# Kernel tuning notes

Hardware: AMD Instinct MI355X
Metric: run time of the kernel (lower is better)

The kernel has to match this reference:

```python
import jax, jax.numpy as jnp
import numpy as np

B, S, N, H, F, L, Lt = 2, 8, 150, 128, 40, 2, 1
EF = 2 * F + 2  # 82: src feat + dst feat + distance + bond
_rows_np, _cols_np = np.where(~np.eye(N, dtype=bool))  # fully connected, no self loops
_rows = jnp.asarray(_rows_np)
_cols = jnp.asarray(_cols_np)
E = _rows_np.shape[0]


def setup_inputs() -> dict:
    key = jax.random.key(0)
    ks = jax.random.split(key, 20)
    w = lambda k, shape: 0.1 * jax.random.normal(k, shape, dtype=jnp.float32)
    d = {}
    d['t'] = jax.random.uniform(ks[0], (B, 1), dtype=jnp.float32)
    d['x'] = jax.random.normal(ks[1], (B, S, N, 3), dtype=jnp.float32)
    d['peptide_seq'] = jax.random.randint(ks[2], (B, 15), 0, 20)
    d['atom_labels'] = jax.random.randint(ks[3], (B, N), 0, 5)
    d['amino_acid_pos'] = jax.random.randint(ks[4], (B, N), 1, 16)
    d['bond_matrix'] = (jax.random.uniform(ks[5], (B, N, N)) < 0.1).astype(jnp.float32)
    d['edge_mask'] = jnp.ones((B, N, N), jnp.float32)
    d['atom_mask'] = jnp.ones((B, N, 1), jnp.float32)
    d['restore_indices'] = jnp.tile(jnp.eye(N, dtype=jnp.float32)[None], (B, 1, 1))
    d['W_e1'] = w(ks[6], (L, EF, H)); d['b_e1'] = jnp.zeros((L, H), jnp.float32)
    d['W_e2'] = w(ks[7], (L, H, H)); d['b_e2'] = jnp.zeros((L, H), jnp.float32)
    d['W_c'] = w(ks[8], (L, H, 1)); d['b_c'] = jnp.zeros((L, 1), jnp.float32)
    d['W_h'] = w(ks[9], (L, F + H, F)); d['b_h'] = jnp.zeros((L, F), jnp.float32)
    d['w_t'] = w(ks[10], (L, 1, H)); d['w_b_t'] = jnp.zeros((L, H), jnp.float32)
    d['tW_e1'] = w(ks[11], (Lt, EF, H)); d['tb_e1'] = jnp.zeros((Lt, H), jnp.float32)
    d['tW_e2'] = w(ks[12], (Lt, H, H)); d['tb_e2'] = jnp.zeros((Lt, H), jnp.float32)
    d['tW_c'] = w(ks[13], (Lt, H, 1)); d['tb_c'] = jnp.zeros((Lt, 1), jnp.float32)
    d['tW_h'] = w(ks[14], (Lt, F + H, F)); d['tb_h'] = jnp.zeros((Lt, F), jnp.float32)
    return d


def _forward(t, x, peptide_seq, atom_labels, amino_acid_pos, bond_matrix, edge_mask,
             atom_mask, restore_indices, W_e1, b_e1, W_e2, b_e2, W_c, b_c, W_h, b_h,
             w_t, w_b_t, tW_e1, tb_e1, tW_e2, tb_e2, tW_c, tb_c, tW_h, tb_h):
    # single-atom embedding: [B, N, 40]
    aa = jnp.take_along_axis(peptide_seq, amino_acid_pos - 1, axis=1)
    emb = jnp.concatenate([
        jax.nn.one_hot(atom_labels, 5, dtype=x.dtype),
        jax.nn.one_hot(aa, 20, dtype=x.dtype),
        jax.nn.one_hot(amino_acid_pos - 1, 15, dtype=x.dtype)], axis=-1)
    h = jnp.broadcast_to(emb[:, None], (B, S, N, F))
    # restore absolute coordinates: x[b,s,i,d] = sum_j x[b,s,j,d] * R[b,i,j]
    x = jnp.einsum('bsjd,bij->bsid', x, restore_indices)
    x0 = x
    # per-edge masks/features (gathered once; identical math to full cdist + indexing)
    em_e = edge_mask.reshape(B, 1, N * N)[:, :, _rows * N + _cols][..., None]  # [B,1,E,1]
    bond_e = jnp.broadcast_to(bond_matrix[:, _rows, _cols][:, None, :, None], (B, S, E, 1))

    def layer(x, h, We1, be1, We2, be2, Wc, bc, Wh, bh, temb):
        diff = x[:, :, _rows] - x[:, :, _cols]                      # [B,S,E,3]
        dist = jnp.sqrt(jnp.sum(diff * diff, -1, keepdims=True) + 1e-12)
        ef = jnp.concatenate([h[:, :, _rows], h[:, :, _cols], dist, bond_e], -1)  # [B,S,E,82]
        m = jax.nn.silu(ef @ We1 + be1 + temb)
        m = jax.nn.silu(m @ We2 + be2) * em_e                        # [B,S,E,H]
        cw = m @ Wc + bc                                             # [B,S,E,1]
        x_out = jnp.zeros_like(x).at[:, :, _rows].add(diff * cw) / (N - 1)
        agg = jnp.zeros((B, S, N, m.shape[-1]), m.dtype).at[:, :, _rows].add(m)
        h_out = jax.nn.silu(jnp.concatenate([h, agg], -1) @ Wh + bh)
        return x_out, h_out

    for l in range(L):
        temb = (t @ w_t[l] + w_b_t[l])[:, None, None, :]             # [B,1,1,H]
        xo, h = layer(x, h, W_e1[l], b_e1[l], W_e2[l], b_e2[l], W_c[l], b_c[l], W_h[l], b_h[l], temb)
        x = x + xo
    for l in range(Lt):
        xo, h = layer(x, h, tW_e1[l], tb_e1[l], tW_e2[l], tb_e2[l], tW_c[l], tb_c[l], tW_h[l], tb_h[l], 0.0)
        x = x + xo
    return (x - x0) * atom_mask[:, None, :, :]


def reference(t, x, peptide_seq, atom_labels, amino_acid_pos, bond_matrix, edge_mask,
              atom_mask, restore_indices, W_e1, b_e1, W_e2, b_e2, W_c, b_c, W_h, b_h,
              w_t, w_b_t, tW_e1, tb_e1, tW_e2, tb_e2, tW_c, tb_c, tW_h, tb_h):
    return _forward(t, x, peptide_seq, atom_labels, amino_acid_pos, bond_matrix, edge_mask,
                    atom_mask, restore_indices, W_e1, b_e1, W_e2, b_e2, W_c, b_c, W_h, b_h,
                    w_t, w_b_t, tW_e1, tb_e1, tW_e2, tb_e2, tW_c, tb_c, tW_h, tb_h)
```

## Files before the change

### kernel.cpp

```cpp
#include <hip/hip_runtime.h>
#include <math.h>

#define B_ 2
#define S_ 8
#define N_ 150
#define H_ 128
#define F_ 40
#define EF_ 82
#define NP_ 160
#define MPQ 136

typedef __attribute__((ext_vector_type(8))) short short8;
typedef __attribute__((ext_vector_type(4))) float float4v;

__device__ __forceinline__ float silu_f(float v) {
    return v * __builtin_amdgcn_rcpf(1.0f + __expf(-v));
}

__device__ __forceinline__ unsigned short f2bf(float f) {
    unsigned u = __builtin_bit_cast(unsigned, f);
    return (unsigned short)((u + 0x7fffu + ((u >> 16) & 1u)) >> 16);
}

__global__ void pack_we2_kernel(const float* __restrict__ w0,
                                const float* __restrict__ w1,
                                const float* __restrict__ w2,
                                unsigned short* __restrict__ outp) {
    int e = blockIdx.x * blockDim.x + threadIdx.x;
    int l = e >> 14, idx = e & 16383;
    int k = idx >> 7, c = idx & 127;
    const float* src = (l == 0) ? w0 : (l == 1) ? w1 : w2;
    outp[l * 16384 + c * H_ + k] = f2bf(src[idx]);
}

__global__ void restore_x_kernel(const float* __restrict__ x,
                                 const float* __restrict__ R,
                                 float* __restrict__ xa,
                                 float* __restrict__ x0) {
    int idx = blockIdx.x * blockDim.x + threadIdx.x;
    if (idx >= B_ * S_ * N_ * 3) return;
    int d = idx % 3;
    int i = (idx / 3) % N_;
    int bs = idx / (3 * N_);
    int b = bs / S_;
    const float* xrow = x + bs * N_ * 3 + d;
    const float* Rrow = R + (b * N_ + i) * N_;
    float acc = 0.0f;
    for (int j = 0; j < N_; j++) acc += xrow[j * 3] * Rrow[j];
    xa[idx] = acc;
    x0[idx] = acc;
}

__global__ void node0_kernel(const int* __restrict__ pep,
                             const int* __restrict__ labels,
                             const int* __restrict__ aapos,
                             const float* __restrict__ We1,
                             const float* __restrict__ be1,
                             const float* __restrict__ tp,
                             const float* __restrict__ wt,
                             const float* __restrict__ wbt,
                             float* __restrict__ h0,
                             float* __restrict__ Af,
                             float* __restrict__ Bf) {
    int bi = blockIdx.x;
    int b = bi / N_, i = bi % N_;
    int c = threadIdx.x;
    int al = labels[bi];
    int ap = aapos[bi];
    int aa = pep[b * 15 + ap - 1];
    int r0 = al, r1 = 5 + aa, r2 = 25 + ap - 1;
    float fa = We1[r0 * H_ + c] + We1[r1 * H_ + c] + We1[r2 * H_ + c]
             + be1[c] + tp[b] * wt[c] + wbt[c];
    float fb = We1[(F_ + r0) * H_ + c] + We1[(F_ + r1) * H_ + c] + We1[(F_ + r2) * H_ + c];
    float hv = 0.0f;
    if (c < F_) hv = (c == r0 || c == r1 || c == r2) ? 1.0f : 0.0f;
    for (int s = 0; s < S_; s++) {
        int n = (b * S_ + s) * N_ + i;
        Af[n * H_ + c] = fa;
        Bf[n * H_ + c] = fb;
        if (c < F_) h0[n * F_ + c] = hv;
    }
}

__global__ void node_kernel(const float* __restrict__ h_in,
                            const float* __restrict__ agg,
                            const float* __restrict__ Wh,
                            const float* __restrict__ bh,
                            const float* __restrict__ We1n,
                            const float* __restrict__ be1n,
                            const float* __restrict__ tp,
                            const float* __restrict__ wtn,
                            const float* __restrict__ wbtn,
                            int has_t,
                            float* __restrict__ h_out,
                            float* __restrict__ Af,
                            float* __restrict__ Bf) {
    int n = blockIdx.x;
    int b = n / (S_ * N_);
    int tid = threadIdx.x;
    __shared__ float cat[F_ + H_];
    __shared__ float part[120];
    __shared__ float hnew[F_];
    if (tid < F_) cat[tid] = h_in[n * F_ + tid];
    cat[F_ + tid] = agg[n * H_ + tid];
    __syncthreads();
    if (tid < 120) {
        int f = tid % 40, ks = tid / 40;
        float p = 0.0f;
        int k0 = ks * 56;
#pragma unroll 8
        for (int k = k0; k < k0 + 56; k++) p += cat[k] * Wh[k * F_ + f];
        part[tid] = p;
    }
    __syncthreads();
    if (tid < F_) {
        float hv = silu_f(part[tid] + part[40 + tid] + part[80 + tid] + bh[tid]);
        hnew[tid] = hv;
        h_out[n * F_ + tid] = hv;
    }
    __syncthreads();
    float fa = be1n[tid] + (has_t ? tp[b] * wtn[tid] + wbtn[tid] : 0.0f);
    float fb = 0.0f;
#pragma unroll 8
    for (int k = 0; k < F_; k++) {
        float hv = hnew[k];
        fa += hv * We1n[k * H_ + tid];
        fb += hv * We1n[(F_ + k) * H_ + tid];
    }
    Af[n * H_ + tid] = fa;
    Bf[n * H_ + tid] = fb;
}

__global__ __launch_bounds__(256, 4) void edge_kernel(
    const float* __restrict__ x_in,
    const float* __restrict__ Afeat,
    const float* __restrict__ Bfeat,
    const float* __restrict__ We1,
    const unsigned short* __restrict__ we2t,
    const float* __restrict__ be2,
    const float* __restrict__ Wc,
    const float* __restrict__ bcp,
    const float* __restrict__ bond,
    const float* __restrict__ emask,
    const float* __restrict__ x0v,
    const float* __restrict__ amask,
    int final_mode,
    float* __restrict__ x_out,
    float* __restrict__ agg_out)
{
    __shared__ __align__(16) short mbuf[2][16 * MPQ];
    __shared__ float4 diffE[NP_];
    __shared__ float2 dbL[NP_];
    __shared__ float DsumL[3];
    __shared__ float wpart[4][3];

    int blk = blockIdx.x;
    int i = blk % N_, bs = blk / N_, b = bs / S_;
    int tid = threadIdx.x;
    int node = bs * N_ + i;
    int lane = tid & 63, w = tid >> 6;
    int qd = lane >> 4, l15 = lane & 15;
    int rowLoc = tid >> 4, c0 = (tid & 15) * 8;

    float xi0 = x_in[node * 3 + 0];
    float xi1 = x_in[node * 3 + 1];
    float xi2 = x_in[node * 3 + 2];

    if (tid < NP_) {
        int j = tid;
        float xj0 = xi0, xj1 = xi1, xj2 = xi2, bnd = 0.0f, emv = 0.0f;
        if (j < N_) {
            int nj = bs * N_ + j;
            xj0 = x_in[nj * 3 + 0];
            xj1 = x_in[nj * 3 + 1];
            xj2 = x_in[nj * 3 + 2];
            int eij = (b * N_ + i) * N_ + j;
            bnd = bond[eij];
            emv = (j == i) ? 0.0f : emask[eij];
        }
        float d0 = xi0 - xj0, d1 = xi1 - xj1, d2 = xi2 - xj2;
        diffE[j] = make_float4(d0, d1, d2, emv);
        dbL[j] = make_float2(sqrtf(d0 * d0 + d1 * d1 + d2 * d2 + 1e-12f), bnd);
    }

    float afr[8], w80r[8], w81r[8];
    {
        float4 t0 = *(const float4*)&Afeat[node * H_ + c0];
        float4 t1 = *(const float4*)&Afeat[node * H_ + c0 + 4];
        afr[0]=t0.x; afr[1]=t0.y; afr[2]=t0.z; afr[3]=t0.w;
        afr[4]=t1.x; afr[5]=t1.y; afr[6]=t1.z; afr[7]=t1.w;
        t0 = *(const float4*)&We1[80 * H_ + c0];
        t1 = *(const float4*)&We1[80 * H_ + c0 + 4];
        w80r[0]=t0.x; w80r[1]=t0.y; w80r[2]=t0.z; w80r[3]=t0.w;
        w80r[4]=t1.x; w80r[5]=t1.y; w80r[6]=t1.z; w80r[7]=t1.w;
        t0 = *(const float4*)&We1[81 * H_ + c0];
        t1 = *(const float4*)&We1[81 * H_ + c0 + 4];
        w81r[0]=t0.x; w81r[1]=t0.y; w81r[2]=t0.z; w81r[3]=t0.w;
        w81r[4]=t1.x; w81r[5]=t1.y; w81r[6]=t1.z; w81r[7]=t1.w;
    }

    int ctb = w * 2;
    float b2r0 = be2[ctb * 16 + l15],  b2r1 = be2[ctb * 16 + 16 + l15];
    float wc0  = Wc[ctb * 16 + l15],   wc1  = Wc[ctb * 16 + 16 + l15];
    const unsigned short* bb0 = we2t + (ctb * 16 + l15) * H_ + qd * 8;
    const unsigned short* bb1 = bb0 + 16 * H_;
    short8 bf00 = *(const short8*)(bb0 +  0);
    short8 bf01 = *(const short8*)(bb0 + 32);
    short8 bf02 = *(const short8*)(bb0 + 64);
    short8 bf03 = *(const short8*)(bb0 + 96);
    short8 bf10 = *(const short8*)(bb1 +  0);
    short8 bf11 = *(const short8*)(bb1 + 32);
    short8 bf12 = *(const short8*)(bb1 + 64);
    short8 bf13 = *(const short8*)(bb1 + 96);

    __syncthreads();

    if (w == 0) {
        float p0 = 0, p1 = 0, p2 = 0;
        for (int j = lane; j < NP_; j += 64) {
            float4 d = diffE[j];
            p0 += d.x; p1 += d.y; p2 += d.z;
        }
        for (int s = 1; s < 64; s <<= 1) {
            p0 += __shfl_xor(p0, s, 64);
            p1 += __shfl_xor(p1, s, 64);
            p2 += __shfl_xor(p2, s, 64);
        }
        if (lane == 0) { DsumL[0] = p0; DsumL[1] = p1; DsumL[2] = p2; }
    }

    float aggP0 = 0, aggP1 = 0;
    float SP00 = 0, SP01 = 0, SP02 = 0, SP10 = 0, SP11 = 0, SP12 = 0;

    for (int jt = 0; jt < 10; jt++) {
        short* mb = mbuf[jt & 1];
        int jrow = jt * 16 + rowLoc;
        float mv[8];
        if (jrow < N_) {
            const float* bp = &Bfeat[(bs * N_ + jrow) * H_ + c0];
            float4 b0 = *(const float4*)bp;
            float4 b1 = *(const float4*)(bp + 4);
            float br[8] = {b0.x, b0.y, b0.z, b0.w, b1.x, b1.y, b1.z, b1.w};
            float2 db = dbL[jrow];
#pragma unroll
            for (int u = 0; u < 8; u++)
                mv[u] = silu_f(afr[u] + br[u] + db.x * w80r[u] + db.y * w81r[u]);
        } else {
#pragma unroll
            for (int u = 0; u < 8; u++) mv[u] = 0.0f;
        }
        short8 pkv;
#pragma unroll
        for (int u = 0; u < 8; u++) pkv[u] = (short)f2bf(mv[u]);
        *(short8*)&mb[rowLoc * MPQ + c0] = pkv;
        __syncthreads();

        const short* arow = &mb[l15 * MPQ + qd * 8];
        short8 a0 = *(const short8*)(arow +  0);
        short8 a1 = *(const short8*)(arow + 32);
        short8 a2 = *(const short8*)(arow + 64);
        short8 a3 = *(const short8*)(arow + 96);
        float4v acc0 = {0, 0, 0, 0}, acc1 = {0, 0, 0, 0};
        acc0 = __builtin_amdgcn_mfma_f32_16x16x32_bf16(a0, bf00, acc0, 0, 0, 0);
        acc1 = __builtin_amdgcn_mfma_f32_16x16x32_bf16(a0, bf10, acc1, 0, 0, 0);
        acc0 = __builtin_amdgcn_mfma_f32_16x16x32_bf16(a1, bf01, acc0, 0, 0, 0);
        acc1 = __builtin_amdgcn_mfma_f32_16x16x32_bf16(a1, bf11, acc1, 0, 0, 0);
        acc0 = __builtin_amdgcn_mfma_f32_16x16x32_bf16(a2, bf02, acc0, 0, 0, 0);
        acc1 = __builtin_amdgcn_mfma_f32_16x16x32_bf16(a2, bf12, acc1, 0, 0, 0);
        acc0 = __builtin_amdgcn_mfma_f32_16x16x32_bf16(a3, bf03, acc0, 0, 0, 0);
        acc1 = __builtin_amdgcn_mfma_f32_16x16x32_bf16(a3, bf13, acc1, 0, 0, 0);

#pragma unroll
        for (int r = 0; r < 4; r++) {
            int j = jt * 16 + qd * 4 + r;
            float4 de = diffE[j];
            float mv0 = silu_f(acc0[r] + b2r0) * de.w;
            float mv1 = silu_f(acc1[r] + b2r1) * de.w;
            aggP0 += mv0; aggP1 += mv1;
            SP00 += de.x * mv0; SP01 += de.y * mv0; SP02 += de.z * mv0;
            SP10 += de.x * mv1; SP11 += de.y * mv1; SP12 += de.z * mv1;
        }
    }

#define QR_(v) { v += __shfl_xor(v, 16, 64); v += __shfl_xor(v, 32, 64); }
    QR_(aggP0) QR_(aggP1)
    QR_(SP00) QR_(SP01) QR_(SP02)
    QR_(SP10) QR_(SP11) QR_(SP12)
#undef QR_

    if (!final_mode && qd == 0) {
        agg_out[node * H_ + ctb * 16 + l15]      = aggP0;
        agg_out[node * H_ + ctb * 16 + 16 + l15] = aggP1;
    }

    float p0 = wc0 * SP00 + wc1 * SP10;
    float p1 = wc0 * SP01 + wc1 * SP11;
    float p2 = wc0 * SP02 + wc1 * SP12;
    for (int s = 1; s < 16; s <<= 1) {
        p0 += __shfl_xor(p0, s, 64);
        p1 += __shfl_xor(p1, s, 64);
        p2 += __shfl_xor(p2, s, 64);
    }
    if (lane == 0) { wpart[w][0] = p0; wpart[w][1] = p1; wpart[w][2] = p2; }
    __syncthreads();
    if (tid < 3) {
        float tot = wpart[0][tid] + wpart[1][tid] + wpart[2][tid] + wpart[3][tid]
                  + bcp[0] * DsumL[tid];
        float xn = x_in[node * 3 + tid] + tot * (1.0f / (float)(N_ - 1));
        if (final_mode)
            x_out[node * 3 + tid] = (xn - x0v[node * 3 + tid]) * amask[b * N_ + i];
        else
            x_out[node * 3 + tid] = xn;
    }
}

extern "C" void kernel_launch(void* const* d_in, const int* in_sizes, int n_in,
                              void* d_out, int out_size, void* d_ws, size_t ws_size,
                              hipStream_t stream) {
    const float* t     = (const float*)d_in[0];
    const float* x     = (const float*)d_in[1];
    const int*   pep   = (const int*)d_in[2];
    const int*   labels= (const int*)d_in[3];
    const int*   aapos = (const int*)d_in[4];
    const float* bond  = (const float*)d_in[5];
    const float* em    = (const float*)d_in[6];
    const float* amask = (const float*)d_in[7];
    const float* R     = (const float*)d_in[8];
    const float* W_e1  = (const float*)d_in[9];
    const float* b_e1  = (const float*)d_in[10];
    const float* W_e2  = (const float*)d_in[11];
    const float* b_e2  = (const float*)d_in[12];
    const float* W_c   = (const float*)d_in[13];
    const float* b_c   = (const float*)d_in[14];
    const float* W_h   = (const float*)d_in[15];
    const float* b_h   = (const float*)d_in[16];
    const float* w_t   = (const float*)d_in[17];
    const float* w_b_t = (const float*)d_in[18];
    const float* tW_e1 = (const float*)d_in[19];
    const float* tb_e1 = (const float*)d_in[20];
    const float* tW_e2 = (const float*)d_in[21];
    const float* tb_e2 = (const float*)d_in[22];
    const float* tW_c  = (const float*)d_in[23];
    const float* tb_c  = (const float*)d_in[24];
    float* out = (float*)d_out;

    float* ws = (float*)d_ws;
    unsigned short* we2t = (unsigned short*)ws;
    float* x0  = ws + 24576;
    float* xA  = x0 + 7200;
    float* xB  = xA + 7200;
    float* hA  = xB + 7200;
    float* hB  = hA + 96000;
    float* agg = hB + 96000;
    float* Af  = agg + 307200;
    float* Bf  = Af + 307200;

    const int XE = B_ * S_ * N_ * 3;
    const int NB = B_ * S_ * N_;

    pack_we2_kernel<<<48, 1024, 0, stream>>>(W_e2, W_e2 + H_ * H_, tW_e2, we2t);
    restore_x_kernel<<<(XE + 255) / 256, 256, 0, stream>>>(x, R, xA, x0);
    node0_kernel<<<B_ * N_, H_, 0, stream>>>(pep, labels, aapos, W_e1, b_e1,
                                             t, w_t, w_b_t, hA, Af, Bf);

    edge_kernel<<<NB, 256, 0, stream>>>(xA, Af, Bf, W_e1, we2t, b_e2, W_c, b_c,
                                        bond, em, nullptr, nullptr, 0, xB, agg);
    node_kernel<<<NB, H_, 0, stream>>>(hA, agg, W_h, b_h,
                                       W_e1 + EF_ * H_, b_e1 + H_,
                                       t, w_t + H_, w_b_t + H_, 1, hB, Af, Bf);

    edge_kernel<<<NB, 256, 0, stream>>>(xB, Af, Bf, W_e1 + EF_ * H_, we2t + 16384,
                                        b_e2 + H_, W_c + H_, b_c + 1,
                                        bond, em, nullptr, nullptr, 0, xA, agg);
    node_kernel<<<NB, H_, 0, stream>>>(hB, agg, W_h + (F_ + H_) * F_, b_h + F_,
                                       tW_e1, tb_e1,
                                       nullptr, nullptr, nullptr, 0, hA, Af, Bf);

    edge_kernel<<<NB, 256, 0, stream>>>(xA, Af, Bf, tW_e1, we2t + 32768,
                                        tb_e2, tW_c, tb_c,
                                        bond, em, x0, amask, 1, out, agg);
}
```

Before: 277.0 us.

## Fuse node update into edge kernel, merge prep kernels, software-pipeline message tiles

Merges the three setup kernels into one prep launch and folds the node MLP (h update and next-layer A/B feature projection) into the tail of each edge kernel. This removes the agg round trip through global memory and several launches. Af/Bf are now double-buffered so that one block's writes cannot race with other blocks still reading the current layer. The edge loop is also software-pipelined: the next 16-row message tile is computed while the MFMAs for the current tile run, leaving one barrier per iteration. The cost is more shared memory and registers per edge block, which may lower occupancy.

```diff
diff --git a/kernel.cpp b/kernel.cpp
--- a/kernel.cpp
+++ b/kernel.cpp
@@ -22,113 +22,63 @@
     return (unsigned short)((u + 0x7fffu + ((u >> 16) & 1u)) >> 16);
 }
 
-__global__ void pack_we2_kernel(const float* __restrict__ w0,
-                                const float* __restrict__ w1,
-                                const float* __restrict__ w2,
-                                unsigned short* __restrict__ outp) {
-    int e = blockIdx.x * blockDim.x + threadIdx.x;
-    int l = e >> 14, idx = e & 16383;
-    int k = idx >> 7, c = idx & 127;
-    const float* src = (l == 0) ? w0 : (l == 1) ? w1 : w2;
-    outp[l * 16384 + c * H_ + k] = f2bf(src[idx]);
-}
-
-__global__ void restore_x_kernel(const float* __restrict__ x,
-                                 const float* __restrict__ R,
-                                 float* __restrict__ xa,
-                                 float* __restrict__ x0) {
-    int idx = blockIdx.x * blockDim.x + threadIdx.x;
-    if (idx >= B_ * S_ * N_ * 3) return;
-    int d = idx % 3;
-    int i = (idx / 3) % N_;
-    int bs = idx / (3 * N_);
-    int b = bs / S_;
-    const float* xrow = x + bs * N_ * 3 + d;
-    const float* Rrow = R + (b * N_ + i) * N_;
-    float acc = 0.0f;
-    for (int j = 0; j < N_; j++) acc += xrow[j * 3] * Rrow[j];
-    xa[idx] = acc;
-    x0[idx] = acc;
-}
-
-__global__ void node0_kernel(const int* __restrict__ pep,
-                             const int* __restrict__ labels,
-                             const int* __restrict__ aapos,
-                             const float* __restrict__ We1,
-                             const float* __restrict__ be1,
-                             const float* __restrict__ tp,
-                             const float* __restrict__ wt,
-                             const float* __restrict__ wbt,
-                             float* __restrict__ h0,
-                             float* __restrict__ Af,
-                             float* __restrict__ Bf) {
-    int bi = blockIdx.x;
-    int b = bi / N_, i = bi % N_;
-    int c = threadIdx.x;
-    int al = labels[bi];
-    int ap = aapos[bi];
-    int aa = pep[b * 15 + ap - 1];
-    int r0 = al, r1 = 5 + aa, r2 = 25 + ap - 1;
-    float fa = We1[r0 * H_ + c] + We1[r1 * H_ + c] + We1[r2 * H_ + c]
-             + be1[c] + tp[b] * wt[c] + wbt[c];
-    float fb = We1[(F_ + r0) * H_ + c] + We1[(F_ + r1) * H_ + c] + We1[(F_ + r2) * H_ + c];
-    float hv = 0.0f;
-    if (c < F_) hv = (c == r0 || c == r1 || c == r2) ? 1.0f : 0.0f;
-    for (int s = 0; s < S_; s++) {
-        int n = (b * S_ + s) * N_ + i;
-        Af[n * H_ + c] = fa;
-        Bf[n * H_ + c] = fb;
-        if (c < F_) h0[n * F_ + c] = hv;
-    }
-}
-
-__global__ void node_kernel(const float* __restrict__ h_in,
-                            const float* __restrict__ agg,
-                            const float* __restrict__ Wh,
-                            const float* __restrict__ bh,
-                            const float* __restrict__ We1n,
-                            const float* __restrict__ be1n,
-                            const float* __restrict__ tp,
-                            const float* __restrict__ wtn,
-                            const float* __restrict__ wbtn,
-                            int has_t,
-                            float* __restrict__ h_out,
-                            float* __restrict__ Af,
-                            float* __restrict__ Bf) {
-    int n = blockIdx.x;
-    int b = n / (S_ * N_);
+__global__ __launch_bounds__(512) void prep_kernel(
+    const float* __restrict__ x, const float* __restrict__ R,
+    const int* __restrict__ pep, const int* __restrict__ labels,
+    const int* __restrict__ aapos,
+    const float* __restrict__ We1, const float* __restrict__ be1,
+    const float* __restrict__ tp, const float* __restrict__ wt,
+    const float* __restrict__ wbt,
+    const float* __restrict__ w2a, const float* __restrict__ w2b,
+    const float* __restrict__ w2c,
+    unsigned short* __restrict__ we2t,
+    float* __restrict__ xa, float* __restrict__ x0,
+    float* __restrict__ h0, float* __restrict__ Af, float* __restrict__ Bf)
+{
+    int blk = blockIdx.x;
     int tid = threadIdx.x;
-    __shared__ float cat[F_ + H_];
-    __shared__ float part[120];
-    __shared__ float hnew[F_];
-    if (tid < F_) cat[tid] = h_in[n * F_ + tid];
-    cat[F_ + tid] = agg[n * H_ + tid];
-    __syncthreads();
-    if (tid < 120) {
-        int f = tid % 40, ks = tid / 40;
-        float p = 0.0f;
-        int k0 = ks * 56;
-#pragma unroll 8
-        for (int k = k0; k < k0 + 56; k++) p += cat[k] * Wh[k * F_ + f];
-        part[tid] = p;
-    }
-    __syncthreads();
-    if (tid < F_) {
-        float hv = silu_f(part[tid] + part[40 + tid] + part[80 + tid] + bh[tid]);
-        hnew[tid] = hv;
-        h_out[n * F_ + tid] = hv;
-    }
-    __syncthreads();
-    float fa = be1n[tid] + (has_t ? tp[b] * wtn[tid] + wbtn[tid] : 0.0f);
-    float fb = 0.0f;
-#pragma unroll 8
-    for (int k = 0; k < F_; k++) {
-        float hv = hnew[k];
-        fa += hv * We1n[k * H_ + tid];
-        fb += hv * We1n[(F_ + k) * H_ + tid];
-    }
-    Af[n * H_ + tid] = fa;
-    Bf[n * H_ + tid] = fb;
+    if (blk < 96) {
+        int e = blk * 512 + tid;
+        int l = e >> 14, idx = e & 16383;
+        int k = idx >> 7, c = idx & 127;
+        const float* src = (l == 0) ? w2a : (l == 1) ? w2b : w2c;
+        we2t[l * 16384 + c * H_ + k] = f2bf(src[idx]);
+    } else if (blk < 112) {
+        int bs = blk - 96;
+        int b = bs / S_;
+        __shared__ float xL[N_ * 3];
+        if (tid < N_ * 3) xL[tid] = x[bs * N_ * 3 + tid];
+        __syncthreads();
+        if (tid < N_ * 3) {
+            int i = tid / 3, d = tid % 3;
+            const float* Rrow = R + (b * N_ + i) * N_;
+            float acc = 0.0f;
+#pragma unroll 5
+            for (int j = 0; j < N_; j++) acc += xL[j * 3 + d] * Rrow[j];
+            xa[bs * N_ * 3 + tid] = acc;
+            x0[bs * N_ * 3 + tid] = acc;
+        }
+    } else {
+        int sub = tid >> 7, c = tid & 127;
+        int bi = (blk - 112) * 4 + sub;
+        int b = bi / N_, i = bi % N_;
+        int al = labels[bi];
+        int ap = aapos[bi];
+        int aa = pep[b * 15 + ap - 1];
+        int r0 = al, r1 = 5 + aa, r2 = 25 + ap - 1;
+        float fa = We1[r0 * H_ + c] + We1[r1 * H_ + c] + We1[r2 * H_ + c]
+                 + be1[c] + tp[b] * wt[c] + wbt[c];
+        float fb = We1[(F_ + r0) * H_ + c] + We1[(F_ + r1) * H_ + c]
+                 + We1[(F_ + r2) * H_ + c];
+        float hv = 0.0f;
+        if (c < F_) hv = (c == r0 || c == r1 || c == r2) ? 1.0f : 0.0f;
+        for (int s = 0; s < S_; s++) {
+            int n = (b * S_ + s) * N_ + i;
+            Af[n * H_ + c] = fa;
+            Bf[n * H_ + c] = fb;
+            if (c < F_) h0[n * F_ + c] = hv;
+        }
+    }
 }
 
 __global__ __launch_bounds__(256, 4) void edge_kernel(
@@ -142,17 +92,31 @@
     const float* __restrict__ bcp,
     const float* __restrict__ bond,
     const float* __restrict__ emask,
+    const float* __restrict__ h_in,
+    const float* __restrict__ Wh,
+    const float* __restrict__ bh,
+    const float* __restrict__ We1n,
+    const float* __restrict__ be1n,
+    const float* __restrict__ tpn,
+    const float* __restrict__ wtn,
+    const float* __restrict__ wbtn,
+    int has_t_next,
     const float* __restrict__ x0v,
     const float* __restrict__ amask,
     int final_mode,
     float* __restrict__ x_out,
-    float* __restrict__ agg_out)
+    float* __restrict__ h_out,
+    float* __restrict__ Af_out,
+    float* __restrict__ Bf_out)
 {
     __shared__ __align__(16) short mbuf[2][16 * MPQ];
     __shared__ float4 diffE[NP_];
     __shared__ float2 dbL[NP_];
     __shared__ float DsumL[3];
     __shared__ float wpart[4][3];
+    __shared__ float cat[F_ + H_];
+    __shared__ float part[160];
+    __shared__ float hnewL[F_];
 
     int blk = blockIdx.x;
     int i = blk % N_, bs = blk / N_, b = bs / S_;
@@ -229,37 +193,40 @@
         if (lane == 0) { DsumL[0] = p0; DsumL[1] = p1; DsumL[2] = p2; }
     }
 
+    {
+        const float* bp = &Bfeat[(bs * N_ + rowLoc) * H_ + c0];
+        float4 b0 = *(const float4*)bp;
+        float4 b1 = *(const float4*)(bp + 4);
+        float br[8] = {b0.x, b0.y, b0.z, b0.w, b1.x, b1.y, b1.z, b1.w};
+        float2 db = dbL[rowLoc];
+        short8 pkv;
+#pragma unroll
+        for (int u = 0; u < 8; u++)
+            pkv[u] = (short)f2bf(silu_f(afr[u] + br[u] + db.x * w80r[u] + db.y * w81r[u]));
+        *(short8*)&mbuf[0][rowLoc * MPQ + c0] = pkv;
+    }
+    __syncthreads();
+
     float aggP0 = 0, aggP1 = 0;
     float SP00 = 0, SP01 = 0, SP02 = 0, SP10 = 0, SP11 = 0, SP12 = 0;
 
+#pragma unroll 2
     for (int jt = 0; jt < 10; jt++) {
         short* mb = mbuf[jt & 1];
-        int jrow = jt * 16 + rowLoc;
-        float mv[8];
-        if (jrow < N_) {
-            const float* bp = &Bfeat[(bs * N_ + jrow) * H_ + c0];
-            float4 b0 = *(const float4*)bp;
-            float4 b1 = *(const float4*)(bp + 4);
-            float br[8] = {b0.x, b0.y, b0.z, b0.w, b1.x, b1.y, b1.z, b1.w};
-            float2 db = dbL[jrow];
-#pragma unroll
-            for (int u = 0; u < 8; u++)
-                mv[u] = silu_f(afr[u] + br[u] + db.x * w80r[u] + db.y * w81r[u]);
-        } else {
-#pragma unroll
-            for (int u = 0; u < 8; u++) mv[u] = 0.0f;
-        }
-        short8 pkv;
-#pragma unroll
-        for (int u = 0; u < 8; u++) pkv[u] = (short)f2bf(mv[u]);
-        *(short8*)&mb[rowLoc * MPQ + c0] = pkv;
-        __syncthreads();
-
         const short* arow = &mb[l15 * MPQ + qd * 8];
         short8 a0 = *(const short8*)(arow +  0);
         short8 a1 = *(const short8*)(arow + 32);
         short8 a2 = *(const short8*)(arow + 64);
         short8 a3 = *(const short8*)(arow + 96);
+
+        int jr = jt * 16 + 16 + rowLoc;
+        float4 nb0 = {0,0,0,0}, nb1 = {0,0,0,0};
+        if (jt < 9 && jr < N_) {
+            const float* bp = &Bfeat[(bs * N_ + jr) * H_ + c0];
+            nb0 = *(const float4*)bp;
+            nb1 = *(const float4*)(bp + 4);
+        }
+
         float4v acc0 = {0, 0, 0, 0}, acc1 = {0, 0, 0, 0};
         acc0 = __builtin_amdgcn_mfma_f32_16x16x32_bf16(a0, bf00, acc0, 0, 0, 0);
         acc1 = __builtin_amdgcn_mfma_f32_16x16x32_bf16(a0, bf10, acc1, 0, 0, 0);
@@ -270,6 +237,21 @@
         acc0 = __builtin_amdgcn_mfma_f32_16x16x32_bf16(a3, bf03, acc0, 0, 0, 0);
         acc1 = __builtin_amdgcn_mfma_f32_16x16x32_bf16(a3, bf13, acc1, 0, 0, 0);
 
+        if (jt < 9) {
+            short8 pkv;
+            if (jr < N_) {
+                float br[8] = {nb0.x, nb0.y, nb0.z, nb0.w, nb1.x, nb1.y, nb1.z, nb1.w};
+                float2 db = dbL[jr];
+#pragma unroll
+                for (int u = 0; u < 8; u++)
+                    pkv[u] = (short)f2bf(silu_f(afr[u] + br[u] + db.x * w80r[u] + db.y * w81r[u]));
+            } else {
+#pragma unroll
+                for (int u = 0; u < 8; u++) pkv[u] = 0;
+            }
+            *(short8*)&mbuf[(jt + 1) & 1][rowLoc * MPQ + c0] = pkv;
+        }
+
 #pragma unroll
         for (int r = 0; r < 4; r++) {
             int j = jt * 16 + qd * 4 + r;
@@ -280,6 +262,7 @@
             SP00 += de.x * mv0; SP01 += de.y * mv0; SP02 += de.z * mv0;
             SP10 += de.x * mv1; SP11 += de.y * mv1; SP12 += de.z * mv1;
         }
+        __syncthreads();
     }
 
 #define QR_(v) { v += __shfl_xor(v, 16, 64); v += __shfl_xor(v, 32, 64); }
@@ -287,11 +270,6 @@
     QR_(SP00) QR_(SP01) QR_(SP02)
     QR_(SP10) QR_(SP11) QR_(SP12)
 #undef QR_
-
-    if (!final_mode && qd == 0) {
-        agg_out[node * H_ + ctb * 16 + l15]      = aggP0;
-        agg_out[node * H_ + ctb * 16 + 16 + l15] = aggP1;
-    }
 
     float p0 = wc0 * SP00 + wc1 * SP10;
     float p1 = wc0 * SP01 + wc1 * SP11;
@@ -302,6 +280,13 @@
         p2 += __shfl_xor(p2, s, 64);
     }
     if (lane == 0) { wpart[w][0] = p0; wpart[w][1] = p1; wpart[w][2] = p2; }
+    if (!final_mode) {
+        if (qd == 0) {
+            cat[F_ + ctb * 16 + l15]      = aggP0;
+            cat[F_ + ctb * 16 + 16 + l15] = aggP1;
+        }
+        if (tid < F_) cat[tid] = h_in[node * F_ + tid];
+    }
     __syncthreads();
     if (tid < 3) {
         float tot = wpart[0][tid] + wpart[1][tid] + wpart[2][tid] + wpart[3][tid]
@@ -311,6 +296,37 @@
             x_out[node * 3 + tid] = (xn - x0v[node * 3 + tid]) * amask[b * N_ + i];
         else
             x_out[node * 3 + tid] = xn;
+    }
+    if (final_mode) return;
+
+    if (tid < 160) {
+        int f = tid >> 2, ks = tid & 3;
+        int k0 = ks * 42;
+        float p = 0.0f;
+#pragma unroll 6
+        for (int k = k0; k < k0 + 42; k++) p += cat[k] * Wh[k * F_ + f];
+        part[tid] = p;
+    }
+    __syncthreads();
+    if (tid < F_) {
+        float hv = silu_f(part[tid * 4] + part[tid * 4 + 1] + part[tid * 4 + 2]
+                        + part[tid * 4 + 3] + bh[tid]);
+        hnewL[tid] = hv;
+        h_out[node * F_ + tid] = hv;
+    }
+    __syncthreads();
+    {
+        int c = tid & 127, grp = tid >> 7;
+        float acc = 0.0f;
+        if (grp == 0) {
+            acc = be1n[c];
+            if (has_t_next) acc += tpn[b] * wtn[c] + wbtn[c];
+        }
+        const float* Wp = We1n + grp * F_ * H_ + c;
+#pragma unroll 8
+        for (int k = 0; k < F_; k++) acc += hnewL[k] * Wp[k * H_];
+        if (grp == 0) Af_out[node * H_ + c] = acc;
+        else          Bf_out[node * H_ + c] = acc;
     }
 }
 
@@ -351,32 +367,33 @@
     float* xB  = xA + 7200;
     float* hA  = xB + 7200;
     float* hB  = hA + 96000;
-    float* agg = hB + 96000;
-    float* Af  = agg + 307200;
-    float* Bf  = Af + 307200;
-
-    const int XE = B_ * S_ * N_ * 3;
+    float* AfA = hB + 96000;
+    float* BfA = AfA + 307200;
+    float* AfB = BfA + 307200;
+    float* BfB = AfB + 307200;
+
     const int NB = B_ * S_ * N_;
 
-    pack_we2_kernel<<<48, 1024, 0, stream>>>(W_e2, W_e2 + H_ * H_, tW_e2, we2t);
-    restore_x_kernel<<<(XE + 255) / 256, 256, 0, stream>>>(x, R, xA, x0);
-    node0_kernel<<<B_ * N_, H_, 0, stream>>>(pep, labels, aapos, W_e1, b_e1,
-                                             t, w_t, w_b_t, hA, Af, Bf);
-
-    edge_kernel<<<NB, 256, 0, stream>>>(xA, Af, Bf, W_e1, we2t, b_e2, W_c, b_c,
-                                        bond, em, nullptr, nullptr, 0, xB, agg);
-    node_kernel<<<NB, H_, 0, stream>>>(hA, agg, W_h, b_h,
-                                       W_e1 + EF_ * H_, b_e1 + H_,
-                                       t, w_t + H_, w_b_t + H_, 1, hB, Af, Bf);
-
-    edge_kernel<<<NB, 256, 0, stream>>>(xB, Af, Bf, W_e1 + EF_ * H_, we2t + 16384,
-                                        b_e2 + H_, W_c + H_, b_c + 1,
-                                        bond, em, nullptr, nullptr, 0, xA, agg);
-    node_kernel<<<NB, H_, 0, stream>>>(hB, agg, W_h + (F_ + H_) * F_, b_h + F_,
-                                       tW_e1, tb_e1,
-                                       nullptr, nullptr, nullptr, 0, hA, Af, Bf);
-
-    edge_kernel<<<NB, 256, 0, stream>>>(xA, Af, Bf, tW_e1, we2t + 32768,
-                                        tb_e2, tW_c, tb_c,
-                                        bond, em, x0, amask, 1, out, agg);
-}
+    prep_kernel<<<187, 512, 0, stream>>>(x, R, pep, labels, aapos,
+                                         W_e1, b_e1, t, w_t, w_b_t,
+                                         W_e2, W_e2 + H_ * H_, tW_e2,
+                                         we2t, xA, x0, hA, AfA, BfA);
+
+    edge_kernel<<<NB, 256, 0, stream>>>(xA, AfA, BfA, W_e1, we2t, b_e2, W_c, b_c,
+        bond, em,
+        hA, W_h, b_h, W_e1 + EF_ * H_, b_e1 + H_, t, w_t + H_, w_b_t + H_, 1,
+        nullptr, nullptr, 0,
+        xB, hB, AfB, BfB);
+
+    edge_kernel<<<NB, 256, 0, stream>>>(xB, AfB, BfB, W_e1 + EF_ * H_, we2t + 16384,
+        b_e2 + H_, W_c + H_, b_c + 1, bond, em,
+        hB, W_h + (F_ + H_) * F_, b_h + F_, tW_e1, tb_e1, nullptr, nullptr, nullptr, 0,
+        nullptr, nullptr, 0,
+        xA, hA, AfA, BfA);
+
+    edge_kernel<<<NB, 256, 0, stream>>>(xA, AfA, BfA, tW_e1, we2t + 32768,
+        tb_e2, tW_c, tb_c, bond, em,
+        nullptr, nullptr, nullptr, nullptr, nullptr, nullptr, nullptr, nullptr, 0,
+        x0, amask, 1,
+        out, nullptr, nullptr, nullptr);
+}
```

Measured after the change: 290.2 us. 4.8% more time.
